# Performance work log

Hardware: AMD Instinct MI355X
Metric: run time of the kernel (lower is better)

The kernel has to match this reference:

```python
import jax, jax.numpy as jnp
import numpy as np
from jax import lax

# ---- constants from init_kwargs (train_coefficients=False -> scalar coeffs) ----
TAU_M, TAU_S = 4.0, 1.0
A1 = float(np.exp(-1.0 / TAU_M) + np.exp(-1.0 / TAU_S))          # IIR feedback coeff 1
A2 = float(-np.exp(-1.0 / TAU_M - 1.0 / TAU_S))                  # IIR feedback coeff 2
ETA = TAU_M / TAU_S
V0 = float(ETA ** (ETA / (ETA - 1.0)) / (ETA - 1.0))             # PSP normalization
SIGMA = float(np.exp(-1.0 / TAU_M))                              # membrane decay
LENGTH = 100
V_TH = 1.0


def dual_exp_iir(x_seq):
    """Dual-exponential synapse as 2nd-order IIR. x_seq: [T, B, F].
    y[t] = A1*y[t-1] + A2*y[t-2] + V0*x[t], zero init states."""
    z = jnp.zeros_like(x_seq[0])
    def step(carry, x_t):
        s1, s2 = carry
        y = A1 * s1 + A2 * s2 + V0 * x_t
        return (y, s1), y
    _, out = lax.scan(step, (z, z), x_seq)
    return out


def spike_fn(v):
    return (v > V_TH).astype(v.dtype)


def neuron_layer(x_seq, w, b):
    """LIF neurons with membrane filter (reset-to-zero on spike).
    x_seq: [T, B, Fin]; w: [Fout, Fin]; b: [Fout]. Returns spikes [T, B, Fout]."""
    cur = jnp.einsum('tbi,oi->tbo', x_seq, w) + b  # batched GEMM over all timesteps
    z = jnp.zeros_like(cur[0])
    def step(carry, c_t):
        v, prev_s = carry
        v_new = SIGMA * v * (1.0 - prev_s) + c_t
        s = spike_fn(v_new)
        return (v_new, s), s
    _, spikes = lax.scan(step, (z, z), cur)
    return spikes


def setup_inputs() -> dict:
    key = jax.random.key(0)
    ks = jax.random.split(key, 7)
    B = 256
    inputs = jax.random.uniform(ks[0], (B, 784), dtype=jnp.float32)
    def lin(k, fo, fi):
        return jax.random.normal(k, (fo, fi), dtype=jnp.float32) / np.sqrt(fi)
    return {
        'inputs': inputs,
        'w1': lin(ks[1], 500, 784), 'b1': jnp.zeros((500,), jnp.float32),
        'w2': lin(ks[2], 500, 500), 'b2': jnp.zeros((500,), jnp.float32),
        'w3': lin(ks[3], 10, 500),  'b3': jnp.zeros((10,), jnp.float32),
    }


def reference(inputs, w1, b1, w2, b2, w3, b3):
    # expand_along_time: [B, 784] -> [T, B, 784] (time-major internally)
    x = jnp.broadcast_to(inputs[None, :, :], (LENGTH,) + inputs.shape)
    h = dual_exp_iir(x)
    s1 = neuron_layer(h, w1, b1)
    h = dual_exp_iir(s1)
    s2 = neuron_layer(h, w2, b2)
    h = dual_exp_iir(s2)
    s3 = neuron_layer(h, w3, b3)            # [T, B, 10]
    return jnp.transpose(s3, (1, 2, 0))     # [B, 10, T] to match torch layout
```

## Files before the change

kernel.cpp:

```cpp
#include <hip/hip_runtime.h>
#include <cstdint>
#include <cstddef>

using f16x8 = __attribute__((ext_vector_type(8))) _Float16;
using f32x4 = __attribute__((ext_vector_type(4))) float;

static constexpr float cA1  =  1.1466802242428472f;
static constexpr float cA2  = -0.2865047968601901f;
static constexpr float cV0  =  2.1165347359575991f;
static constexpr float cSIG =  0.7788007830714049f;

#define TSTEPS 100
#define BATCH  256
#define KPAD   512
#define MROWS  (TSTEPS * BATCH)
#define KS1    7

__device__ __forceinline__ void gload_lds16(const void* g, void* l) {
  __builtin_amdgcn_global_load_lds(
      (void __attribute__((address_space(1)))*)g,
      (void __attribute__((address_space(3)))*)l, 16, 0, 0);
}

__global__ void split_w2(const float* __restrict__ w2,
                         _Float16* __restrict__ Wh, _Float16* __restrict__ Wl) {
  int idx = blockIdx.x * 256 + threadIdx.x;
  int n = idx >> 9, k = idx & 511;
  float x = (n < 500 && k < 500) ? w2[n * 500 + k] : 0.f;
  _Float16 h = (_Float16)x;
  float r = x - (float)h;
  _Float16 l = (_Float16)(r * 4096.f);
  Wh[idx] = h; Wl[idx] = l;
}

#define BM1 64
#define BN1 64
#define BK1 32
#define LDT1 68

__global__ __launch_bounds__(256)
void gemm1_splitk(const float* __restrict__ A, const float* __restrict__ B,
                  float* __restrict__ P) {
  constexpr int M = 256, N = 500, K = 784;
  __shared__ float As[BK1][LDT1];
  __shared__ float Bs[BK1][LDT1];
  const int tid = threadIdx.x;
  const int bm  = blockIdx.y * BM1;
  const int bn  = blockIdx.x * BN1;
  const int ks  = blockIdx.z;
  const int k_begin = ks * 128;
  const int k_end   = (k_begin + 128 < K) ? k_begin + 128 : K;
  const int tr  = tid >> 4;
  const int tc  = tid & 15;
  float acc[4][4] = {{0.f}};

  for (int k0 = k_begin; k0 < k_end; k0 += BK1) {
#pragma unroll
    for (int i = 0; i < 2; ++i) {
      const int t = tid + i * 256;
      const int r = t >> 3;
      const int c = (t & 7) << 2;
      const int gk = k0 + c;
      float4 va = make_float4(0.f, 0.f, 0.f, 0.f);
      const int gm = bm + r;
      if (gm < M && gk < k_end) {
        if (gk + 3 < k_end) va = *(const float4*)(A + (size_t)gm * K + gk);
        else {
          const float* p = A + (size_t)gm * K;
          va.x = p[gk];
          if (gk + 1 < k_end) va.y = p[gk + 1];
          if (gk + 2 < k_end) va.z = p[gk + 2];
        }
      }
      As[c + 0][r] = va.x; As[c + 1][r] = va.y;
      As[c + 2][r] = va.z; As[c + 3][r] = va.w;
      float4 vb = make_float4(0.f, 0.f, 0.f, 0.f);
      const int gn = bn + r;
      if (gn < N && gk < k_end) {
        if (gk + 3 < k_end) vb = *(const float4*)(B + (size_t)gn * K + gk);
        else {
          const float* p = B + (size_t)gn * K;
          vb.x = p[gk];
          if (gk + 1 < k_end) vb.y = p[gk + 1];
          if (gk + 2 < k_end) vb.z = p[gk + 2];
        }
      }
      Bs[c + 0][r] = vb.x; Bs[c + 1][r] = vb.y;
      Bs[c + 2][r] = vb.z; Bs[c + 3][r] = vb.w;
    }
    __syncthreads();
#pragma unroll
    for (int kk = 0; kk < BK1; ++kk) {
      const float4 a = *(const float4*)&As[kk][tr * 4];
      const float4 b = *(const float4*)&Bs[kk][tc * 4];
      acc[0][0] += a.x * b.x; acc[0][1] += a.x * b.y; acc[0][2] += a.x * b.z; acc[0][3] += a.x * b.w;
      acc[1][0] += a.y * b.x; acc[1][1] += a.y * b.y; acc[1][2] += a.y * b.z; acc[1][3] += a.y * b.w;
      acc[2][0] += a.z * b.x; acc[2][1] += a.z * b.y; acc[2][2] += a.z * b.z; acc[2][3] += a.z * b.w;
      acc[3][0] += a.w * b.x; acc[3][1] += a.w * b.y; acc[3][2] += a.w * b.z; acc[3][3] += a.w * b.w;
    }
    __syncthreads();
  }
#pragma unroll
  for (int i = 0; i < 4; ++i) {
    const int m = bm + tr * 4 + i;
#pragma unroll
    for (int j = 0; j < 4; ++j) {
      const int n = bn + tc * 4 + j;
      if (n < N) P[((size_t)ks * 256 + m) * 512 + n] = acc[i][j];
    }
  }
}

__global__ __launch_bounds__(256)
void layer1_split(const float* __restrict__ P,
                  const float* __restrict__ b1,
                  _Float16* __restrict__ Ah,
                  _Float16* __restrict__ Al) {
  int idx = blockIdx.x * 256 + threadIdx.x;
  int b = idx >> 9, o = idx & 511;
  if (o >= 500) {
    for (int t = 0; t < TSTEPS; ++t) {
      size_t off = (size_t)(t * BATCH + b) * KPAD + o;
      Ah[off] = (_Float16)0; Al[off] = (_Float16)0;
    }
    return;
  }
  float g = 0.f;
  for (int ks = 0; ks < KS1; ++ks)
    g += P[((size_t)ks * 256 + b) * 512 + o];
  const float bb = b1[o];
  float v = 0.f, sp = 0.f, y1 = 0.f, y2 = 0.f;
  float c1 = 0.f, c2 = 0.f;
  for (int t = 0; t < TSTEPS; ++t) {
    float c = cA1 * c1 + cA2 * c2 + cV0; c2 = c1; c1 = c;
    float cur = c * g + bb;
    float vv = cSIG * v * (1.f - sp) + cur;
    float s = (vv > 1.f) ? 1.f : 0.f;
    v = vv; sp = s;
    float y = cA1 * y1 + cA2 * y2 + cV0 * s;
    y2 = y1; y1 = y;
    _Float16 h = (_Float16)y;
    float r = y - (float)h;
    size_t off = (size_t)(t * BATCH + b) * KPAD + o;
    Ah[off] = h;
    Al[off] = (_Float16)(r * 4096.f);
  }
}

__global__ __launch_bounds__(512, 2)
void gemm2_f16(const _Float16* __restrict__ Ah, const _Float16* __restrict__ Al,
               const _Float16* __restrict__ Bh, const _Float16* __restrict__ Bl,
               const float* __restrict__ bias, float* __restrict__ C) {
  __shared__ char smem[2][4][16384];
  const int tid  = threadIdx.x;
  const int lane = tid & 63;
  const int wid  = tid >> 6;
  const int wr   = wid >> 2;
  const int wc   = wid & 3;
  const int g    = blockIdx.x;
  const int wg   = (g & 7) * 25 + (g >> 3);
  const int bm   = wg * 128;
  const int lrow = lane & 15;
  const int lkc  = lane >> 4;

  auto stage = [&](int buf, int step) {
    const int k0 = (step & 7) * 64;
    const int bn = (step >> 3) * 128;
#pragma unroll
    for (int i = 0; i < 2; ++i) {
      const int l = i * 8192 + tid * 16;
      const int row = l >> 7;
      const int chunk = ((l >> 4) & 7) ^ (row & 7);
      const size_t ga = (size_t)(bm + row) * KPAD + k0 + chunk * 8;
      const size_t gb = (size_t)(bn + row) * KPAD + k0 + chunk * 8;
      gload_lds16(Ah + ga, &smem[buf][0][l]);
      gload_lds16(Al + ga, &smem[buf][1][l]);
      gload_lds16(Bh + gb, &smem[buf][2][l]);
      gload_lds16(Bl + gb, &smem[buf][3][l]);
    }
  };

  stage(0, 0);
  asm volatile("s_waitcnt vmcnt(0)" ::: "memory");
  __builtin_amdgcn_s_barrier();

#pragma unroll 1
  for (int job = 0; job < 4; ++job) {
    f32x4 acc0[4][2], acc1[4][2];
#pragma unroll
    for (int m = 0; m < 4; ++m)
#pragma unroll
      for (int n = 0; n < 2; ++n) {
        acc0[m][n] = (f32x4){0.f, 0.f, 0.f, 0.f};
        acc1[m][n] = (f32x4){0.f, 0.f, 0.f, 0.f};
      }

#pragma unroll 1
    for (int T = 0; T < 8; ++T) {
      const int step = job * 8 + T;
      const int cur  = step & 1;
      if (step < 31) stage(cur ^ 1, step + 1);

      const char* sAh = smem[cur][0];
      const char* sAl = smem[cur][1];
      const char* sBh = smem[cur][2];
      const char* sBl = smem[cur][3];
#pragma unroll
      for (int kh = 0; kh < 2; ++kh) {
        const int kc = kh * 4 + lkc;
        f16x8 ah[4], al[4];
#pragma unroll
        for (int m = 0; m < 4; ++m) {
          const int row = wr * 64 + m * 16 + lrow;
          const int off = row * 128 + ((kc ^ (row & 7)) << 4);
          ah[m] = *(const f16x8*)(sAh + off);
          al[m] = *(const f16x8*)(sAl + off);
        }
#pragma unroll
        for (int n = 0; n < 2; ++n) {
          const int row = wc * 32 + n * 16 + lrow;
          const int off = row * 128 + ((kc ^ (row & 7)) << 4);
          f16x8 bh = *(const f16x8*)(sBh + off);
          f16x8 bl = *(const f16x8*)(sBl + off);
#pragma unroll
          for (int m = 0; m < 4; ++m) {
            acc0[m][n] = __builtin_amdgcn_mfma_f32_16x16x32_f16(ah[m], bh, acc0[m][n], 0, 0, 0);
            acc1[m][n] = __builtin_amdgcn_mfma_f32_16x16x32_f16(ah[m], bl, acc1[m][n], 0, 0, 0);
            acc1[m][n] = __builtin_amdgcn_mfma_f32_16x16x32_f16(al[m], bh, acc1[m][n], 0, 0, 0);
          }
        }
      }
      asm volatile("s_waitcnt vmcnt(0)" ::: "memory");
      __builtin_amdgcn_s_barrier();
    }

    const int bn = job * 128;
#pragma unroll
    for (int m = 0; m < 4; ++m) {
      const int gm0 = bm + wr * 64 + m * 16 + (lane >> 4) * 4;
#pragma unroll
      for (int n = 0; n < 2; ++n) {
        const int gn = bn + wc * 32 + n * 16 + (lane & 15);
        const float bs = (gn < 500) ? bias[gn] : 0.f;
#pragma unroll
        for (int r = 0; r < 4; ++r)
          C[(size_t)(gm0 + r) * KPAD + gn] =
              acc0[m][n][r] + 0.000244140625f * acc1[m][n][r] + bs;
      }
    }
  }
}

__global__ __launch_bounds__(256)
void lif_mid(float* __restrict__ q) {
  int idx = blockIdx.x * 256 + threadIdx.x;
  int b = idx >> 9, o = idx & 511;
  if (o >= 500) return;
  float v = 0.f, sp = 0.f, y1 = 0.f, y2 = 0.f;
  for (int t = 0; t < TSTEPS; ++t) {
    size_t off = (size_t)(t * BATCH + b) * KPAD + o;
    float qv = q[off];
    float vv = cSIG * v * (1.f - sp) + qv;
    float s = (vv > 1.f) ? 1.f : 0.f;
    v = vv; sp = s;
    float y = cA1 * y1 + cA2 * y2 + cV0 * s;
    y2 = y1; y1 = y;
    q[off] = y;
  }
}

__global__ __launch_bounds__(256)
void gemm3_wave(const float* __restrict__ y, const float* __restrict__ w3,
                float* __restrict__ q3) {
  __shared__ float ws3[10 * 500];
  for (int i = threadIdx.x; i < 5000; i += 256) ws3[i] = w3[i];
  __syncthreads();
  const int wid = threadIdx.x >> 6, lane = threadIdx.x & 63;
  const int m = blockIdx.x * 4 + wid;
  float p[10];
#pragma unroll
  for (int o = 0; o < 10; ++o) p[o] = 0.f;
  for (int k = lane; k < 500; k += 64) {
    float h = y[(size_t)m * KPAD + k];
#pragma unroll
    for (int o = 0; o < 10; ++o) p[o] += h * ws3[o * 500 + k];
  }
#pragma unroll
  for (int o = 0; o < 10; ++o) {
    float v = p[o];
    for (int off = 32; off; off >>= 1) v += __shfl_down(v, off, 64);
    if (lane == 0) q3[(size_t)m * 10 + o] = v;
  }
}

__global__ __launch_bounds__(64)
void lif_out3(const float* __restrict__ q,
              const float* __restrict__ b3,
              float* __restrict__ out) {
  int idx = blockIdx.x * 64 + threadIdx.x;
  if (idx >= BATCH * 10) return;
  int b = idx / 10, o = idx - b * 10;
  float bb = b3[o];
  float v = 0.f, sp = 0.f;
  for (int t = 0; t < TSTEPS; ++t) {
    float cur = q[(size_t)(t * BATCH + b) * 10 + o] + bb;
    float vv = cSIG * v * (1.f - sp) + cur;
    float s = (vv > 1.f) ? 1.f : 0.f;
    v = vv; sp = s;
    out[(size_t)b * 1000 + (size_t)o * 100 + t] = s;
  }
}

extern "C" void kernel_launch(void* const* d_in, const int* in_sizes, int n_in,
                              void* d_out, int out_size, void* d_ws, size_t ws_size,
                              hipStream_t stream) {
  const float* inputs = (const float*)d_in[0];
  const float* w1 = (const float*)d_in[1];
  const float* b1 = (const float*)d_in[2];
  const float* w2 = (const float*)d_in[3];
  const float* b2 = (const float*)d_in[4];
  const float* w3 = (const float*)d_in[5];
  const float* b3 = (const float*)d_in[6];
  float* out = (float*)d_out;

  char* ws = (char*)d_ws;
  _Float16* w2h = (_Float16*)ws; ws += 512 * 512 * 2;
  _Float16* w2l = (_Float16*)ws; ws += 512 * 512 * 2;
  float* P1 = (float*)ws;        ws += (size_t)KS1 * 256 * 512 * 4;
  float* q2 = (float*)ws;        ws += (size_t)MROWS * KPAD * 4;
  float* q3 = (float*)ws;        ws += (size_t)MROWS * 10 * 4;
  _Float16* Ah = (_Float16*)ws;  ws += (size_t)MROWS * KPAD * 2;
  _Float16* Al = (_Float16*)ws;  ws += (size_t)MROWS * KPAD * 2;

  split_w2<<<dim3(512 * 512 / 256), dim3(256), 0, stream>>>(w2, w2h, w2l);

  gemm1_splitk<<<dim3(8, 4, KS1), dim3(256), 0, stream>>>(inputs, w1, P1);
  layer1_split<<<dim3(BATCH * 512 / 256), dim3(256), 0, stream>>>(P1, b1, Ah, Al);

  gemm2_f16<<<dim3(200), dim3(512), 0, stream>>>(Ah, Al, w2h, w2l, b2, q2);
  lif_mid<<<dim3(BATCH * 512 / 256), dim3(256), 0, stream>>>(q2);

  gemm3_wave<<<dim3(MROWS / 4), dim3(256), 0, stream>>>(q2, w3, q3);
  lif_out3<<<dim3((BATCH * 10 + 63) / 64), dim3(64), 0, stream>>>(q3, b3, out);
}
```

Baseline: 148.1 us.

## Triple-buffer gemm2 K-loop with BK=32 and fuse w2 split into gemm1

```diff
diff --git a/kernel.cpp b/kernel.cpp
--- a/kernel.cpp
+++ b/kernel.cpp
@@ -22,17 +22,6 @@
       (void __attribute__((address_space(3)))*)l, 16, 0, 0);
 }
 
-__global__ void split_w2(const float* __restrict__ w2,
-                         _Float16* __restrict__ Wh, _Float16* __restrict__ Wl) {
-  int idx = blockIdx.x * 256 + threadIdx.x;
-  int n = idx >> 9, k = idx & 511;
-  float x = (n < 500 && k < 500) ? w2[n * 500 + k] : 0.f;
-  _Float16 h = (_Float16)x;
-  float r = x - (float)h;
-  _Float16 l = (_Float16)(r * 4096.f);
-  Wh[idx] = h; Wl[idx] = l;
-}
-
 #define BM1 64
 #define BN1 64
 #define BK1 32
@@ -40,8 +29,22 @@
 
 __global__ __launch_bounds__(256)
 void gemm1_splitk(const float* __restrict__ A, const float* __restrict__ B,
-                  float* __restrict__ P) {
+                  float* __restrict__ P,
+                  const float* __restrict__ w2,
+                  _Float16* __restrict__ Wh, _Float16* __restrict__ Wl) {
   constexpr int M = 256, N = 500, K = 784;
+  if (blockIdx.z == KS1) {
+    int base = (blockIdx.x + blockIdx.y * 8) * 256 + threadIdx.x;
+    for (int idx = base; idx < 512 * 512; idx += 32 * 256) {
+      int n = idx >> 9, k = idx & 511;
+      float x = (n < 500 && k < 500) ? w2[n * 500 + k] : 0.f;
+      _Float16 h = (_Float16)x;
+      float r = x - (float)h;
+      Wh[idx] = h;
+      Wl[idx] = (_Float16)(r * 4096.f);
+    }
+    return;
+  }
   __shared__ float As[BK1][LDT1];
   __shared__ float Bs[BK1][LDT1];
   const int tid = threadIdx.x;
@@ -151,101 +154,99 @@
 void gemm2_f16(const _Float16* __restrict__ Ah, const _Float16* __restrict__ Al,
                const _Float16* __restrict__ Bh, const _Float16* __restrict__ Bl,
                const float* __restrict__ bias, float* __restrict__ C) {
-  __shared__ char smem[2][4][16384];
+  __shared__ char smem[3 * 32768];
   const int tid  = threadIdx.x;
   const int lane = tid & 63;
   const int wid  = tid >> 6;
   const int wr   = wid >> 2;
   const int wc   = wid & 3;
-  const int g    = blockIdx.x;
-  const int wg   = (g & 7) * 25 + (g >> 3);
+  const int orig = blockIdx.x;
+  const int wg   = (orig & 7) * 25 + (orig >> 3);
   const int bm   = wg * 128;
   const int lrow = lane & 15;
   const int lkc  = lane >> 4;
 
-  auto stage = [&](int buf, int step) {
-    const int k0 = (step & 7) * 64;
-    const int bn = (step >> 3) * 128;
-#pragma unroll
-    for (int i = 0; i < 2; ++i) {
-      const int l = i * 8192 + tid * 16;
-      const int row = l >> 7;
-      const int chunk = ((l >> 4) & 7) ^ (row & 7);
-      const size_t ga = (size_t)(bm + row) * KPAD + k0 + chunk * 8;
-      const size_t gb = (size_t)(bn + row) * KPAD + k0 + chunk * 8;
-      gload_lds16(Ah + ga, &smem[buf][0][l]);
-      gload_lds16(Al + ga, &smem[buf][1][l]);
-      gload_lds16(Bh + gb, &smem[buf][2][l]);
-      gload_lds16(Bl + gb, &smem[buf][3][l]);
-    }
+  auto stage = [&](int buf, int v) {
+    const int k0 = (v & 15) * 32;
+    const int bn = (v >> 4) * 128;
+    char* base = smem + buf * 32768;
+    const int l = tid * 16;
+    const int row = l >> 6;
+    const int chunk = ((l >> 4) & 3) ^ ((row >> 1) & 3);
+    const size_t ga = (size_t)(bm + row) * KPAD + k0 + chunk * 8;
+    const size_t gb = (size_t)(bn + row) * KPAD + k0 + chunk * 8;
+    gload_lds16(Ah + ga, base + l);
+    gload_lds16(Al + ga, base + 8192 + l);
+    gload_lds16(Bh + gb, base + 16384 + l);
+    gload_lds16(Bl + gb, base + 24576 + l);
   };
 
+  f32x4 acc0[4][2], acc1[4][2];
+#pragma unroll
+  for (int m = 0; m < 4; ++m)
+#pragma unroll
+    for (int n = 0; n < 2; ++n) {
+      acc0[m][n] = (f32x4){0.f, 0.f, 0.f, 0.f};
+      acc1[m][n] = (f32x4){0.f, 0.f, 0.f, 0.f};
+    }
+
   stage(0, 0);
-  asm volatile("s_waitcnt vmcnt(0)" ::: "memory");
-  __builtin_amdgcn_s_barrier();
+  stage(1, 1);
 
 #pragma unroll 1
-  for (int job = 0; job < 4; ++job) {
-    f32x4 acc0[4][2], acc1[4][2];
-#pragma unroll
-    for (int m = 0; m < 4; ++m)
-#pragma unroll
-      for (int n = 0; n < 2; ++n) {
-        acc0[m][n] = (f32x4){0.f, 0.f, 0.f, 0.f};
-        acc1[m][n] = (f32x4){0.f, 0.f, 0.f, 0.f};
+  for (int v = 0; v < 64; ++v) {
+    if (v < 63) asm volatile("s_waitcnt vmcnt(4)" ::: "memory");
+    else        asm volatile("s_waitcnt vmcnt(0)" ::: "memory");
+    __builtin_amdgcn_s_barrier();
+    __builtin_amdgcn_sched_barrier(0);
+
+    if (v + 2 < 64) stage((v + 2) % 3, v + 2);
+    __builtin_amdgcn_sched_barrier(0);
+
+    const char* base = smem + (v % 3) * 32768;
+    f16x8 ah[4], al[4];
+#pragma unroll
+    for (int m = 0; m < 4; ++m) {
+      const int row = wr * 64 + m * 16 + lrow;
+      const int off = row * 64 + ((lkc ^ ((row >> 1) & 3)) << 4);
+      ah[m] = *(const f16x8*)(base + off);
+      al[m] = *(const f16x8*)(base + 8192 + off);
+    }
+    f16x8 bh[2], bl[2];
+#pragma unroll
+    for (int n = 0; n < 2; ++n) {
+      const int row = wc * 32 + n * 16 + lrow;
+      const int off = row * 64 + ((lkc ^ ((row >> 1) & 3)) << 4);
+      bh[n] = *(const f16x8*)(base + 16384 + off);
+      bl[n] = *(const f16x8*)(base + 24576 + off);
+    }
+    __builtin_amdgcn_s_setprio(1);
+#pragma unroll
+    for (int n = 0; n < 2; ++n)
+#pragma unroll
+      for (int m = 0; m < 4; ++m) {
+        acc0[m][n] = __builtin_amdgcn_mfma_f32_16x16x32_f16(ah[m], bh[n], acc0[m][n], 0, 0, 0);
+        acc1[m][n] = __builtin_amdgcn_mfma_f32_16x16x32_f16(ah[m], bl[n], acc1[m][n], 0, 0, 0);
+        acc1[m][n] = __builtin_amdgcn_mfma_f32_16x16x32_f16(al[m], bh[n], acc1[m][n], 0, 0, 0);
       }
-
-#pragma unroll 1
-    for (int T = 0; T < 8; ++T) {
-      const int step = job * 8 + T;
-      const int cur  = step & 1;
-      if (step < 31) stage(cur ^ 1, step + 1);
-
-      const char* sAh = smem[cur][0];
-      const char* sAl = smem[cur][1];
-      const char* sBh = smem[cur][2];
-      const char* sBl = smem[cur][3];
-#pragma unroll
-      for (int kh = 0; kh < 2; ++kh) {
-        const int kc = kh * 4 + lkc;
-        f16x8 ah[4], al[4];
-#pragma unroll
-        for (int m = 0; m < 4; ++m) {
-          const int row = wr * 64 + m * 16 + lrow;
-          const int off = row * 128 + ((kc ^ (row & 7)) << 4);
-          ah[m] = *(const f16x8*)(sAh + off);
-          al[m] = *(const f16x8*)(sAl + off);
+    __builtin_amdgcn_s_setprio(0);
+
+    if ((v & 15) == 15) {
+      const int bn = (v >> 4) * 128;
+#pragma unroll
+      for (int m = 0; m < 4; ++m) {
+        const int gm0 = bm + wr * 64 + m * 16 + (lane >> 4) * 4;
+#pragma unroll
+        for (int n = 0; n < 2; ++n) {
+          const int gn = bn + wc * 32 + n * 16 + (lane & 15);
+          const float bs = (gn < 500) ? bias[gn] : 0.f;
+#pragma unroll
+          for (int r = 0; r < 4; ++r)
+            C[(size_t)(gm0 + r) * KPAD + gn] =
+                acc0[m][n][r] + 0.000244140625f * acc1[m][n][r] + bs;
+          acc0[m][n] = (f32x4){0.f, 0.f, 0.f, 0.f};
+          acc1[m][n] = (f32x4){0.f, 0.f, 0.f, 0.f};
         }
-#pragma unroll
-        for (int n = 0; n < 2; ++n) {
-          const int row = wc * 32 + n * 16 + lrow;
-          const int off = row * 128 + ((kc ^ (row & 7)) << 4);
-          f16x8 bh = *(const f16x8*)(sBh + off);
-          f16x8 bl = *(const f16x8*)(sBl + off);
-#pragma unroll
-          for (int m = 0; m < 4; ++m) {
-            acc0[m][n] = __builtin_amdgcn_mfma_f32_16x16x32_f16(ah[m], bh, acc0[m][n], 0, 0, 0);
-            acc1[m][n] = __builtin_amdgcn_mfma_f32_16x16x32_f16(ah[m], bl, acc1[m][n], 0, 0, 0);
-            acc1[m][n] = __builtin_amdgcn_mfma_f32_16x16x32_f16(al[m], bh, acc1[m][n], 0, 0, 0);
-          }
-        }
-      }
-      asm volatile("s_waitcnt vmcnt(0)" ::: "memory");
-      __builtin_amdgcn_s_barrier();
-    }
-
-    const int bn = job * 128;
-#pragma unroll
-    for (int m = 0; m < 4; ++m) {
-      const int gm0 = bm + wr * 64 + m * 16 + (lane >> 4) * 4;
-#pragma unroll
-      for (int n = 0; n < 2; ++n) {
-        const int gn = bn + wc * 32 + n * 16 + (lane & 15);
-        const float bs = (gn < 500) ? bias[gn] : 0.f;
-#pragma unroll
-        for (int r = 0; r < 4; ++r)
-          C[(size_t)(gm0 + r) * KPAD + gn] =
-              acc0[m][n][r] + 0.000244140625f * acc1[m][n][r] + bs;
       }
     }
   }
@@ -332,9 +333,8 @@
   _Float16* Ah = (_Float16*)ws;  ws += (size_t)MROWS * KPAD * 2;
   _Float16* Al = (_Float16*)ws;  ws += (size_t)MROWS * KPAD * 2;
 
-  split_w2<<<dim3(512 * 512 / 256), dim3(256), 0, stream>>>(w2, w2h, w2l);
-
-  gemm1_splitk<<<dim3(8, 4, KS1), dim3(256), 0, stream>>>(inputs, w1, P1);
+  gemm1_splitk<<<dim3(8, 4, KS1 + 1), dim3(256), 0, stream>>>(
+      inputs, w1, P1, w2, w2h, w2l);
   layer1_split<<<dim3(BATCH * 512 / 256), dim3(256), 0, stream>>>(P1, b1, Ah, Al);
 
   gemm2_f16<<<dim3(200), dim3(512), 0, stream>>>(Ah, Al, w2h, w2l, b2, q2);
```

Measured after the change: 148.8 us. No clear change (+0.5%).
